# Kernel optimization log

Measured on AMD Instinct MI355X. Metric: run time of the kernel, lower is better.

The kernel has to match this reference:

```python
import jax, jax.numpy as jnp
import numpy as np

B_SZ, N_NODES, C_IN, C_OUT, M_EDGES, DEG = 32, 4096, 64, 64, 64, 256
E_INC = M_EDGES * DEG  # 16384 incidences
NEG_SLOPE = 0.2
MARGIN = 4.2


def setup_inputs() -> dict:
    key = jax.random.key(0)
    k1, k2, k3, k4 = jax.random.split(key, 4)
    x = jax.random.normal(k1, (B_SZ, N_NODES, C_IN), jnp.float32)
    # glorot-ish params
    weight = jax.random.normal(k2, (C_IN, C_OUT), jnp.float32) * (1.0 / np.sqrt(C_IN))
    att = jax.random.normal(k3, (1, 1, 2 * C_OUT), jnp.float32) * 0.1
    node_ids = jax.random.randint(k4, (E_INC,), 0, N_NODES, dtype=jnp.int32)
    edge_ids = jnp.repeat(jnp.arange(M_EDGES, dtype=jnp.int32), DEG)  # sorted, all edges present
    hyperedge_index = jnp.stack([node_ids, edge_ids], axis=0)
    return {"x": x, "weight": weight, "att": att,
            "hyperedge_index": hyperedge_index,
            "num_edges": M_EDGES, "num_nodes": N_NODES}


def _segment_softmax(scores, seg, num_segments):
    m = jax.ops.segment_max(scores, seg, num_segments=num_segments)
    e = jnp.exp(scores - m[seg])
    s = jax.ops.segment_sum(e, seg, num_segments=num_segments)
    return e / s[seg]


def reference(x, weight, att, hyperedge_index, num_edges, num_nodes):
    node_ids = hyperedge_index[0]
    edge_ids = hyperedge_index[1]
    M = num_edges
    N = num_nodes

    xw = jnp.einsum('bnc,cd->bnd', x, weight)       # [B,N,C]
    x1 = jnp.swapaxes(xw, 0, 1)                     # [N,B,C]

    x_i = x1[node_ids]                              # [E,B,C] gather per incidence
    edge_sums = jax.ops.segment_sum(x_i, edge_ids, num_segments=M,
                                    indices_are_sorted=True)  # [M,B,C]
    x_j = edge_sums[edge_ids]                       # [E,B,C]

    # pairwise hyperedge contrastive loss (vectorized double loop over edges)
    inner = jnp.einsum('kbc,mbc->kmb', edge_sums, edge_sums)          # [M,M,B]
    nrm = jnp.linalg.norm(edge_sums, axis=-1)                         # [M,B]
    cos = inner / (nrm[:, None, :] * nrm[None, :, :])                 # [M,M,B]
    diff = edge_sums[:, None] - edge_sums[None, :]                    # [M,M,B,C]
    dist = jnp.linalg.norm(diff, axis=-1)                             # [M,M,B]
    loss_item = cos * dist + (1.0 - cos) * jnp.clip(MARGIN - dist, 0.0)
    loss_hyper = jnp.sum(jnp.abs(jnp.mean(loss_item, axis=2))) / (M + 1) ** 2

    # GAT-style attention over incidences, softmax grouped by node
    cat = jnp.concatenate([x_i, x_j], axis=-1)                        # [E,B,2C]
    scores = jnp.sum(cat * att[0], axis=-1)                           # [E,B] (heads=1)
    scores = jax.nn.leaky_relu(scores, negative_slope=NEG_SLOPE)
    alpha = _segment_softmax(scores, node_ids, N)                     # [E,B]
    # dropout omitted (eval mode)

    ones = jnp.ones((node_ids.shape[0],), xw.dtype)
    D = jax.ops.segment_sum(ones, node_ids, num_segments=N)           # node degree
    deg_e = jax.ops.segment_sum(ones, edge_ids, num_segments=M, indices_are_sorted=True)
    B_norm = jnp.where(deg_e > 0, 1.0 / deg_e, 0.0)                   # 1/edge degree, inf->0

    # stage 1: nodes -> hyperedges (source_to_target)
    msg1 = B_norm[edge_ids][:, None, None] * (alpha[..., None] * x_i) # [E,B,C]
    out_e = jax.ops.segment_sum(msg1, edge_ids, num_segments=M, indices_are_sorted=True)
    # stage 2: hyperedges -> nodes (target_to_source)
    msg2 = D[node_ids][:, None, None] * (alpha[..., None] * out_e[edge_ids])
    out_n = jax.ops.segment_sum(msg2, node_ids, num_segments=N)       # [N,B,C]

    out = jnp.swapaxes(out_n, 0, 1)                                   # [B,N,C]
    constrain_total = jnp.abs(jnp.mean(x_i - x_j)) + loss_hyper
    return out, constrain_total
```

## Files before the change

kernel.cpp:

```cpp
#include <hip/hip_runtime.h>
#include <math.h>

#define B_SZ 32
#define N_NODES 4096
#define C_DIM 64
#define M_EDGES 64
#define DEG 256
#define E_INC 16384
#define NEG_SLOPE 0.2f
#define MARGIN 4.2f

__device__ __forceinline__ float wsum64(float v) {
#pragma unroll
  for (int off = 32; off > 0; off >>= 1) v += __shfl_xor(v, off, 64);
  return v;
}

__device__ __forceinline__ float4 redq16_32(float4 a) {
#pragma unroll
  for (int off = 16; off < 64; off <<= 1) {
    a.x += __shfl_xor(a.x, off, 64);
    a.y += __shfl_xor(a.y, off, 64);
    a.z += __shfl_xor(a.z, off, 64);
    a.w += __shfl_xor(a.w, off, 64);
  }
  return a;
}

#define ACC4(acc, v)  \
  acc.x += v.x;       \
  acc.y += v.y;       \
  acc.z += v.z;       \
  acc.w += v.w;

#define FMA4(acc, a, v)        \
  acc.x = fmaf(a, v.x, acc.x); \
  acc.y = fmaf(a, v.y, acc.y); \
  acc.z = fmaf(a, v.z, acc.z); \
  acc.w = fmaf(a, v.w, acc.w);

union U16K {
  float wl[4096];
  int cnt[4096];
};

__global__ __launch_bounds__(256) void k_pA(
    const float* __restrict__ x, const float* __restrict__ w,
    const float* __restrict__ att, const int* __restrict__ node_ids,
    float* __restrict__ s1_t, float* __restrict__ es_t,
    float* __restrict__ s2, float* __restrict__ nrm2,
    float* __restrict__ essum, int* __restrict__ cntv) {
  __shared__ U16K u;
  __shared__ float sx[4][4][64];
  __shared__ float est[4][64];
  const int bid = blockIdx.x;
  const int t = threadIdx.x;
  const int lane = t & 63, wv = t >> 6;
  if (bid < 512) {
    __shared__ float part[4][64];
    __shared__ float wattl[64];
    const int kk = t & 63, q = t >> 6;
    float p = 0.f;
#pragma unroll
    for (int c = 0; c < 16; ++c)
      p = fmaf(w[kk * 64 + q * 16 + c], att[q * 16 + c], p);
    part[q][kk] = p;
    __syncthreads();
    if (t < 64)
      wattl[t] = part[0][t] + part[1][t] + part[2][t] + part[3][t];
    __syncthreads();
    const int kq = lane & 15, rsub = lane >> 4;
    const float4 wq = ((const float4*)wattl)[kq];
    const int r0 = bid * 256 + wv * 64;
#pragma unroll 4
    for (int it = 0; it < 16; ++it) {
      const int row = r0 + it * 4 + rsub;
      const float4 xv = ((const float4*)x)[row * 16 + kq];
      float vv = xv.x * wq.x + xv.y * wq.y + xv.z * wq.z + xv.w * wq.w;
      vv += __shfl_xor(vv, 1, 64);
      vv += __shfl_xor(vv, 2, 64);
      vv += __shfl_xor(vv, 4, 64);
      vv += __shfl_xor(vv, 8, 64);
      if (kq == 0) {
        const int n = row & (N_NODES - 1);
        const int b = row >> 12;
        s1_t[n * 32 + b] = vv;
      }
    }
  } else if (bid < 576) {
    const int m = bid - 512;
#pragma unroll
    for (int i = 0; i < 16; ++i) u.cnt[t + 256 * i] = 0;
    __syncthreads();
    atomicAdd(&u.cnt[node_ids[m * DEG + t]], 1);
    __syncthreads();
#pragma unroll
    for (int i = 0; i < 16; ++i)
      cntv[m * N_NODES + t + 256 * i] = u.cnt[t + 256 * i];
  } else {
    const int eb = bid - 576;
    const int b0 = (eb & 7) * 4;
    const int m = eb >> 3;
    const int qc = lane & 15, rg = lane >> 4;
    float4* wl4 = (float4*)u.wl;
    const float4* w4 = (const float4*)w;
#pragma unroll
    for (int i = 0; i < 4; ++i) wl4[t + 256 * i] = w4[t + 256 * i];
    const int myinc = node_ids[m * DEG + wv * 64 + lane];
    int nds[16];
#pragma unroll
    for (int i = 0; i < 16; ++i) nds[i] = __shfl(myinc, i * 4 + rg, 64);
#pragma unroll
    for (int p = 0; p < 2; ++p) {
      const float4* xA =
          (const float4*)(x + (size_t)(b0 + 2 * p) * (N_NODES * C_DIM));
      const float4* xB =
          (const float4*)(x + (size_t)(b0 + 2 * p + 1) * (N_NODES * C_DIM));
      float4 vA[8], vB[8];
#pragma unroll
      for (int j = 0; j < 8; ++j) vA[j] = xA[nds[j] * 16 + qc];
#pragma unroll
      for (int j = 0; j < 8; ++j) vB[j] = xB[nds[j] * 16 + qc];
      float4 aA = {0.f, 0.f, 0.f, 0.f}, aB = {0.f, 0.f, 0.f, 0.f};
#pragma unroll
      for (int j = 0; j < 8; ++j) { ACC4(aA, vA[j]); }
#pragma unroll
      for (int j = 0; j < 8; ++j) vA[j] = xA[nds[8 + j] * 16 + qc];
#pragma unroll
      for (int j = 0; j < 8; ++j) { ACC4(aB, vB[j]); }
#pragma unroll
      for (int j = 0; j < 8; ++j) vB[j] = xB[nds[8 + j] * 16 + qc];
#pragma unroll
      for (int j = 0; j < 8; ++j) { ACC4(aA, vA[j]); }
#pragma unroll
      for (int j = 0; j < 8; ++j) { ACC4(aB, vB[j]); }
      aA = redq16_32(aA);
      aB = redq16_32(aB);
      if (rg == 0) {
        ((float4*)&sx[wv][2 * p][0])[qc] = aA;
        ((float4*)&sx[wv][2 * p + 1][0])[qc] = aB;
      }
    }
    __syncthreads();
    {
      const int c = lane;
      float es = 0.f;
#pragma unroll 8
      for (int j = 0; j < 64; ++j) {
        const float sxcj =
            sx[0][wv][j] + sx[1][wv][j] + sx[2][wv][j] + sx[3][wv][j];
        es = fmaf(sxcj, u.wl[j * 64 + c], es);
      }
      est[wv][c] = es;
      const float sr = wsum64(es * att[64 + c]);
      const float nr = wsum64(es * es);
      const float er = wsum64(es);
      if (c == 0) {
        s2[m * 32 + b0 + wv] = sr;
        nrm2[m * 32 + b0 + wv] = nr;
        essum[m * 32 + b0 + wv] = er;
      }
    }
    __syncthreads();
    if (t < 64) {
      const float4 o = make_float4(est[0][t], est[1][t], est[2][t], est[3][t]);
      *(float4*)&es_t[(m * 64 + t) * 32 + b0] = o;
    }
  }
}

__global__ __launch_bounds__(256) void k_pB(
    const float* __restrict__ es_t, const float* __restrict__ nrm2,
    const int* __restrict__ cntv, const float* __restrict__ s1_t,
    const float* __restrict__ s2, float* __restrict__ lossbuf2,
    float2* __restrict__ pnb, int* __restrict__ pdat,
    int* __restrict__ plen) {
  const int bid = blockIdx.x;
  if (bid < 504) {
    const int wv = threadIdx.x >> 6;
    const int p = bid * 4 + wv;
    int k = 0, off = 0;
    while (off + (63 - k) <= p) {
      off += 63 - k;
      ++k;
    }
    const int m = k + 1 + (p - off);
    const int lane = threadIdx.x & 63;
    const int b = lane & 31, ch = lane >> 5;
    float inner = 0.f;
#pragma unroll 8
    for (int cc = 0; cc < 32; ++cc) {
      const int c = cc + 32 * ch;
      inner = fmaf(es_t[(k * 64 + c) * 32 + b], es_t[(m * 64 + c) * 32 + b],
                   inner);
    }
    inner += __shfl_xor(inner, 32, 64);
    const float nk2 = nrm2[k * 32 + b];
    const float nm2 = nrm2[m * 32 + b];
    const float d2 = fmaxf(nk2 + nm2 - 2.f * inner, 0.f);
    const float dist = sqrtf(d2);
    const float cosv = inner / sqrtf(nk2 * nm2);
    float li = cosv * dist + (1.f - cosv) * fmaxf(MARGIN - dist, 0.f);
#pragma unroll
    for (int o = 16; o > 0; o >>= 1) li += __shfl_xor(li, o, 64);
    if (lane == 0) lossbuf2[p] = 2.f * fabsf(li * (1.f / 32.f));
  } else {
    const int idx = (bid - 504) * 256 + threadIdx.x;
    const int n = idx >> 5, b = idx & 31;
    const float s1v = s1_t[n * 32 + b];
    const bool leader = (b == 0);
    float mx = -1e30f, S = 0.f;
    int j = 0, Dsum = 0;
#pragma unroll 4
    for (int m = 0; m < 64; ++m) {
      const int cm = cntv[m * N_NODES + n];
      float sc = s1v + s2[m * 32 + b];
      sc = sc > 0.f ? sc : NEG_SLOPE * sc;
      const float scv = (cm > 0) ? sc : -1e30f;
      const float nm = fmaxf(mx, scv);
      S = S * __expf(mx - nm) + (float)cm * __expf(scv - nm);
      mx = nm;
      if (leader) {
        if (cm > 0) {
          pdat[n * 64 + j] = m | (cm << 8);
          ++j;
        }
        Dsum += cm;
      }
    }
    if (leader) plen[n] = j | (Dsum << 7);
    float2 pv;
    pv.x = mx;
    pv.y = (S > 0.f) ? 1.f / S : 0.f;
    pnb[n * 32 + b] = pv;
  }
}

__global__ __launch_bounds__(256) void k_pC(
    const float* __restrict__ x, const int* __restrict__ node_ids,
    const float* __restrict__ w, const float* __restrict__ s1_t,
    const float* __restrict__ s2, const float2* __restrict__ pnb,
    const float* __restrict__ essum, const float* __restrict__ lossbuf2,
    float* __restrict__ out_e_t, float* __restrict__ outs) {
  __shared__ float wl[4096];
  __shared__ float sx[4][4][64];
  __shared__ float est[4][64];
  const int bid = blockIdx.x;
  const int t = threadIdx.x;
  if (bid < 512) {
    const int b0 = (bid & 7) * 4;
    const int m = bid >> 3;
    const int lane = t & 63, wv = t >> 6;
    const int qc = lane & 15, rg = lane >> 4;
    float4* wl4 = (float4*)wl;
    const float4* w4 = (const float4*)w;
#pragma unroll
    for (int i = 0; i < 4; ++i) wl4[t + 256 * i] = w4[t + 256 * i];
    const int myinc = node_ids[m * DEG + wv * 64 + lane];
    const float4 s14 = *(const float4*)&s1_t[myinc * 32 + b0];
    const float* pp = (const float*)&pnb[myinc * 32 + b0];
    const float4 pA = *(const float4*)pp;
    const float4 pB = *(const float4*)(pp + 4);
    float mya[4];
    {
      const float s1a[4] = {s14.x, s14.y, s14.z, s14.w};
      const float mxa[4] = {pA.x, pA.z, pB.x, pB.z};
      const float iva[4] = {pA.y, pA.w, pB.y, pB.w};
#pragma unroll
      for (int bi = 0; bi < 4; ++bi) {
        float sc = s1a[bi] + s2[m * 32 + b0 + bi];
        sc = sc > 0.f ? sc : NEG_SLOPE * sc;
        mya[bi] = __expf(sc - mxa[bi]) * iva[bi];
      }
    }
    int nds[16];
#pragma unroll
    for (int i = 0; i < 16; ++i) nds[i] = __shfl(myinc, i * 4 + rg, 64);
#pragma unroll
    for (int p = 0; p < 2; ++p) {
      const float4* xA =
          (const float4*)(x + (size_t)(b0 + 2 * p) * (N_NODES * C_DIM));
      const float4* xB =
          (const float4*)(x + (size_t)(b0 + 2 * p + 1) * (N_NODES * C_DIM));
      float avA[16], avB[16];
#pragma unroll
      for (int i = 0; i < 16; ++i) {
        avA[i] = __shfl(mya[2 * p], i * 4 + rg, 64);
        avB[i] = __shfl(mya[2 * p + 1], i * 4 + rg, 64);
      }
      float4 vA[8], vB[8];
#pragma unroll
      for (int j = 0; j < 8; ++j) vA[j] = xA[nds[j] * 16 + qc];
#pragma unroll
      for (int j = 0; j < 8; ++j) vB[j] = xB[nds[j] * 16 + qc];
      float4 aA = {0.f, 0.f, 0.f, 0.f}, aB = {0.f, 0.f, 0.f, 0.f};
#pragma unroll
      for (int j = 0; j < 8; ++j) { FMA4(aA, avA[j], vA[j]); }
#pragma unroll
      for (int j = 0; j < 8; ++j) vA[j] = xA[nds[8 + j] * 16 + qc];
#pragma unroll
      for (int j = 0; j < 8; ++j) { FMA4(aB, avB[j], vB[j]); }
#pragma unroll
      for (int j = 0; j < 8; ++j) vB[j] = xB[nds[8 + j] * 16 + qc];
#pragma unroll
      for (int j = 0; j < 8; ++j) { FMA4(aA, avA[8 + j], vA[j]); }
#pragma unroll
      for (int j = 0; j < 8; ++j) { FMA4(aB, avB[8 + j], vB[j]); }
      aA = redq16_32(aA);
      aB = redq16_32(aB);
      if (rg == 0) {
        ((float4*)&sx[wv][2 * p][0])[qc] = aA;
        ((float4*)&sx[wv][2 * p + 1][0])[qc] = aB;
      }
    }
    __syncthreads();
    {
      const int c = t & 63;
      const int wv2 = t >> 6;
      float oc = 0.f;
#pragma unroll 8
      for (int j = 0; j < 64; ++j) {
        const float sxcj =
            sx[0][wv2][j] + sx[1][wv2][j] + sx[2][wv2][j] + sx[3][wv2][j];
        oc = fmaf(sxcj, wl[j * 64 + c], oc);
      }
      est[wv2][c] = oc * (1.0f / 256.0f);
    }
    __syncthreads();
    if (t < 64) {
      const float4 o = make_float4(est[0][t], est[1][t], est[2][t], est[3][t]);
      *(float4*)&out_e_t[(m * 64 + t) * 32 + b0] = o;
    }
  } else {
    __shared__ float smf[256];
    float s = 0.f;
    for (int i = t; i < M_EDGES * B_SZ; i += 256) s += essum[i];
    smf[t] = s;
    __syncthreads();
    for (int o = 128; o > 0; o >>= 1) {
      if (t < o) smf[t] += smf[t + o];
      __syncthreads();
    }
    const float S = smf[0];
    __syncthreads();
    float l = 0.f;
    for (int i = t; i < 2016; i += 256) l += lossbuf2[i];
    smf[t] = l;
    __syncthreads();
    for (int o = 128; o > 0; o >>= 1) {
      if (t < o) smf[t] += smf[t + o];
      __syncthreads();
    }
    if (t == 0) {
      const float mean = S * (-255.0f) / 33554432.0f;
      outs[0] = fabsf(mean) + smf[0] * (1.0f / 4225.0f);
    }
  }
}

__global__ __launch_bounds__(256) void k_pD(
    const int* __restrict__ plen, const int* __restrict__ pdat,
    const float* __restrict__ s1_t, const float* __restrict__ s2,
    const float2* __restrict__ pnb, const float* __restrict__ out_e_t,
    float* __restrict__ out) {
  __shared__ int lme[2][64];
  __shared__ float lcnt[2][64];
  __shared__ float al[2][64][32];
  const int t = threadIdx.x;
  const int nd = t >> 7;
  const int n = blockIdx.x * 2 + nd;
  const int tl = t & 127;
  const int pl = plen[n];
  const int len = pl & 127;
  const float Dn = (float)(pl >> 7);
  if (tl < len) {
    const int pe = pdat[n * 64 + tl];
    lme[nd][tl] = pe & 63;
    lcnt[nd][tl] = (float)(pe >> 8);
  }
  __syncthreads();
  {
    const int b = tl & 31, lq = tl >> 5;
    const float s1v = s1_t[n * 32 + b];
    const float2 pv = pnb[n * 32 + b];
    for (int base = 0; base < len; base += 4) {
      const int li = base + lq;
      if (li < len) {
        const int m = lme[nd][li];
        float sc = s1v + s2[m * 32 + b];
        sc = sc > 0.f ? sc : NEG_SLOPE * sc;
        al[nd][li][b] = lcnt[nd][li] * __expf(sc - pv.x) * pv.y;
      }
    }
  }
  __syncthreads();
  const int c = tl & 63, bh = tl >> 6;
  float4 a0 = {0.f, 0.f, 0.f, 0.f}, a1 = {0.f, 0.f, 0.f, 0.f};
  float4 a2 = {0.f, 0.f, 0.f, 0.f}, a3 = {0.f, 0.f, 0.f, 0.f};
  for (int li = 0; li < len; ++li) {
    const int m = lme[nd][li];
    const float* ob = &out_e_t[(m * 64 + c) * 32 + bh * 16];
    const float4 v0 = *(const float4*)(ob);
    const float4 v1 = *(const float4*)(ob + 4);
    const float4 v2 = *(const float4*)(ob + 8);
    const float4 v3 = *(const float4*)(ob + 12);
    const float* alr = &al[nd][li][bh * 16];
    a0.x = fmaf(alr[0], v0.x, a0.x);
    a0.y = fmaf(alr[1], v0.y, a0.y);
    a0.z = fmaf(alr[2], v0.z, a0.z);
    a0.w = fmaf(alr[3], v0.w, a0.w);
    a1.x = fmaf(alr[4], v1.x, a1.x);
    a1.y = fmaf(alr[5], v1.y, a1.y);
    a1.z = fmaf(alr[6], v1.z, a1.z);
    a1.w = fmaf(alr[7], v1.w, a1.w);
    a2.x = fmaf(alr[8], v2.x, a2.x);
    a2.y = fmaf(alr[9], v2.y, a2.y);
    a2.z = fmaf(alr[10], v2.z, a2.z);
    a2.w = fmaf(alr[11], v2.w, a2.w);
    a3.x = fmaf(alr[12], v3.x, a3.x);
    a3.y = fmaf(alr[13], v3.y, a3.y);
    a3.z = fmaf(alr[14], v3.z, a3.z);
    a3.w = fmaf(alr[15], v3.w, a3.w);
  }
  const size_t nb = (size_t)n * 64 + c;
  const size_t st = (size_t)N_NODES * 64;
  const int bb = bh * 16;
  out[(bb + 0) * st + nb] = Dn * a0.x;
  out[(bb + 1) * st + nb] = Dn * a0.y;
  out[(bb + 2) * st + nb] = Dn * a0.z;
  out[(bb + 3) * st + nb] = Dn * a0.w;
  out[(bb + 4) * st + nb] = Dn * a1.x;
  out[(bb + 5) * st + nb] = Dn * a1.y;
  out[(bb + 6) * st + nb] = Dn * a1.z;
  out[(bb + 7) * st + nb] = Dn * a1.w;
  out[(bb + 8) * st + nb] = Dn * a2.x;
  out[(bb + 9) * st + nb] = Dn * a2.y;
  out[(bb + 10) * st + nb] = Dn * a2.z;
  out[(bb + 11) * st + nb] = Dn * a2.w;
  out[(bb + 12) * st + nb] = Dn * a3.x;
  out[(bb + 13) * st + nb] = Dn * a3.y;
  out[(bb + 14) * st + nb] = Dn * a3.z;
  out[(bb + 15) * st + nb] = Dn * a3.w;
}

extern "C" void kernel_launch(void* const* d_in, const int* in_sizes, int n_in,
                              void* d_out, int out_size, void* d_ws,
                              size_t ws_size, hipStream_t stream) {
  (void)in_sizes; (void)n_in; (void)out_size; (void)ws_size;
  const float* x = (const float*)d_in[0];
  const float* weight = (const float*)d_in[1];
  const float* att = (const float*)d_in[2];
  const int* node_ids = (const int*)d_in[3];
  float* out = (float*)d_out;

  char* wsb = (char*)d_ws;
  float* es_t = (float*)(wsb);
  float* out_e_t = (float*)(wsb + (512 << 10));
  float* s1_t = (float*)(wsb + (1024 << 10));
  int* cntv = (int*)(wsb + (1536 << 10));
  float2* pnb = (float2*)(wsb + (2560 << 10));
  int* pdat = (int*)(wsb + (3584 << 10));
  float* s2 = (float*)(wsb + (4608 << 10));
  float* nrm2 = (float*)(wsb + (4616 << 10));
  float* essum = (float*)(wsb + (4624 << 10));
  float* lossbuf2 = (float*)(wsb + (4632 << 10));
  int* plen = (int*)(wsb + (4640 << 10));

  k_pA<<<1088, 256, 0, stream>>>(x, weight, att, node_ids, s1_t, es_t, s2,
                                 nrm2, essum, cntv);
  k_pB<<<1016, 256, 0, stream>>>(es_t, nrm2, cntv, s1_t, s2, lossbuf2, pnb,
                                 pdat, plen);
  k_pC<<<513, 256, 0, stream>>>(x, node_ids, weight, s1_t, s2, pnb, essum,
                                lossbuf2, out_e_t,
                                out + (size_t)B_SZ * N_NODES * C_DIM);
  k_pD<<<2048, 256, 0, stream>>>(plen, pdat, s1_t, s2, pnb, out_e_t, out);
}
```

Before: 82.12 us.

## Replace edge-side gather with node-major scatter into LDS partials plus reduce kernel

The stage-1 aggregation (nodes to hyperedges) no longer gathers x rows per incidence. Each block now streams contiguous node rows for one batch and scatters alpha-weighted values into per-wave LDS accumulators indexed by edge, using the per-node compressed edge lists built earlier. A new kernel sums the 16 chunk partials and applies the weight matrix. The aim is to swap random gathers of x for coalesced reads. The cost is an extra launch, a 4 MB partial buffer written and read back, and LDS read-modify-write traffic that can hit bank conflicts.

```diff
diff --git a/kernel.cpp b/kernel.cpp
--- a/kernel.cpp
+++ b/kernel.cpp
@@ -27,17 +27,11 @@
   return a;
 }
 
-#define ACC4(acc, v)  \
-  acc.x += v.x;       \
-  acc.y += v.y;       \
-  acc.z += v.z;       \
+#define ACC4(acc, v) \
+  acc.x += v.x;      \
+  acc.y += v.y;      \
+  acc.z += v.z;      \
   acc.w += v.w;
-
-#define FMA4(acc, a, v)        \
-  acc.x = fmaf(a, v.x, acc.x); \
-  acc.y = fmaf(a, v.y, acc.y); \
-  acc.z = fmaf(a, v.z, acc.z); \
-  acc.w = fmaf(a, v.w, acc.w);
 
 union U16K {
   float wl[4096];
@@ -236,100 +230,73 @@
   }
 }
 
-__global__ __launch_bounds__(256) void k_pC(
-    const float* __restrict__ x, const int* __restrict__ node_ids,
-    const float* __restrict__ w, const float* __restrict__ s1_t,
+__global__ __launch_bounds__(256) void k_pC1(
+    const float* __restrict__ x, const float* __restrict__ s1_t,
     const float* __restrict__ s2, const float2* __restrict__ pnb,
+    const int* __restrict__ plen, const int* __restrict__ pdat,
     const float* __restrict__ essum, const float* __restrict__ lossbuf2,
-    float* __restrict__ out_e_t, float* __restrict__ outs) {
-  __shared__ float wl[4096];
-  __shared__ float sx[4][4][64];
-  __shared__ float est[4][64];
+    float* __restrict__ partialT, float* __restrict__ outs) {
   const int bid = blockIdx.x;
   const int t = threadIdx.x;
   if (bid < 512) {
-    const int b0 = (bid & 7) * 4;
-    const int m = bid >> 3;
-    const int lane = t & 63, wv = t >> 6;
-    const int qc = lane & 15, rg = lane >> 4;
-    float4* wl4 = (float4*)wl;
-    const float4* w4 = (const float4*)w;
-#pragma unroll
-    for (int i = 0; i < 4; ++i) wl4[t + 256 * i] = w4[t + 256 * i];
-    const int myinc = node_ids[m * DEG + wv * 64 + lane];
-    const float4 s14 = *(const float4*)&s1_t[myinc * 32 + b0];
-    const float* pp = (const float*)&pnb[myinc * 32 + b0];
-    const float4 pA = *(const float4*)pp;
-    const float4 pB = *(const float4*)(pp + 4);
-    float mya[4];
-    {
-      const float s1a[4] = {s14.x, s14.y, s14.z, s14.w};
-      const float mxa[4] = {pA.x, pA.z, pB.x, pB.z};
-      const float iva[4] = {pA.y, pA.w, pB.y, pB.w};
-#pragma unroll
-      for (int bi = 0; bi < 4; ++bi) {
-        float sc = s1a[bi] + s2[m * 32 + b0 + bi];
-        sc = sc > 0.f ? sc : NEG_SLOPE * sc;
-        mya[bi] = __expf(sc - mxa[bi]) * iva[bi];
-      }
-    }
-    int nds[16];
-#pragma unroll
-    for (int i = 0; i < 16; ++i) nds[i] = __shfl(myinc, i * 4 + rg, 64);
-#pragma unroll
-    for (int p = 0; p < 2; ++p) {
-      const float4* xA =
-          (const float4*)(x + (size_t)(b0 + 2 * p) * (N_NODES * C_DIM));
-      const float4* xB =
-          (const float4*)(x + (size_t)(b0 + 2 * p + 1) * (N_NODES * C_DIM));
-      float avA[16], avB[16];
-#pragma unroll
-      for (int i = 0; i < 16; ++i) {
-        avA[i] = __shfl(mya[2 * p], i * 4 + rg, 64);
-        avB[i] = __shfl(mya[2 * p + 1], i * 4 + rg, 64);
-      }
-      float4 vA[8], vB[8];
-#pragma unroll
-      for (int j = 0; j < 8; ++j) vA[j] = xA[nds[j] * 16 + qc];
-#pragma unroll
-      for (int j = 0; j < 8; ++j) vB[j] = xB[nds[j] * 16 + qc];
-      float4 aA = {0.f, 0.f, 0.f, 0.f}, aB = {0.f, 0.f, 0.f, 0.f};
-#pragma unroll
-      for (int j = 0; j < 8; ++j) { FMA4(aA, avA[j], vA[j]); }
-#pragma unroll
-      for (int j = 0; j < 8; ++j) vA[j] = xA[nds[8 + j] * 16 + qc];
-#pragma unroll
-      for (int j = 0; j < 8; ++j) { FMA4(aB, avB[j], vB[j]); }
-#pragma unroll
-      for (int j = 0; j < 8; ++j) vB[j] = xB[nds[8 + j] * 16 + qc];
-#pragma unroll
-      for (int j = 0; j < 8; ++j) { FMA4(aA, avA[8 + j], vA[j]); }
-#pragma unroll
-      for (int j = 0; j < 8; ++j) { FMA4(aB, avB[8 + j], vB[j]); }
-      aA = redq16_32(aA);
-      aB = redq16_32(aB);
-      if (rg == 0) {
-        ((float4*)&sx[wv][2 * p][0])[qc] = aA;
-        ((float4*)&sx[wv][2 * p + 1][0])[qc] = aB;
-      }
-    }
-    __syncthreads();
-    {
-      const int c = t & 63;
-      const int wv2 = t >> 6;
-      float oc = 0.f;
-#pragma unroll 8
-      for (int j = 0; j < 64; ++j) {
-        const float sxcj =
-            sx[0][wv2][j] + sx[1][wv2][j] + sx[2][wv2][j] + sx[3][wv2][j];
-        oc = fmaf(sxcj, wl[j * 64 + c], oc);
-      }
-      est[wv2][c] = oc * (1.0f / 256.0f);
-    }
-    __syncthreads();
-    if (t < 64) {
-      const float4 o = make_float4(est[0][t], est[1][t], est[2][t], est[3][t]);
-      *(float4*)&out_e_t[(m * 64 + t) * 32 + b0] = o;
+    __shared__ float Tw[4][64][64];
+    const int b = bid & 31;
+    const int ch = bid >> 5;
+    const int c = t & 63, wv = t >> 6;
+    float* tz = &Tw[0][0][0];
+    for (int i = t; i < 4 * 64 * 64; i += 256) tz[i] = 0.f;
+    __syncthreads();
+    const int nbase = ch * 256 + wv * 64;
+    const float* xb = x + (size_t)b * (N_NODES * C_DIM);
+#pragma unroll 1
+    for (int g = 0; g < 16; ++g) {
+      const int n0 = nbase + g * 4;
+      float xv[4], s1v[4];
+      int pl[4];
+      float2 pv[4];
+      int4 pd0[4], pd1[4];
+#pragma unroll
+      for (int u = 0; u < 4; ++u) {
+        const int n = n0 + u;
+        xv[u] = xb[n * 64 + c];
+        pl[u] = plen[n];
+        s1v[u] = s1_t[n * 32 + b];
+        pv[u] = pnb[n * 32 + b];
+        pd0[u] = *(const int4*)&pdat[n * 64];
+        pd1[u] = *(const int4*)&pdat[n * 64 + 4];
+      }
+#pragma unroll
+      for (int u = 0; u < 4; ++u) {
+        const int len = pl[u] & 127;
+        const int pes[8] = {pd0[u].x, pd0[u].y, pd0[u].z, pd0[u].w,
+                            pd1[u].x, pd1[u].y, pd1[u].z, pd1[u].w};
+#pragma unroll
+        for (int j = 0; j < 8; ++j) {
+          if (j < len) {
+            const int pe = pes[j];
+            const int m = pe & 63;
+            float sc = s1v[u] + s2[m * 32 + b];
+            sc = sc > 0.f ? sc : NEG_SLOPE * sc;
+            const float a =
+                (float)(pe >> 8) * __expf(sc - pv[u].x) * pv[u].y;
+            Tw[wv][m][c] += a * xv[u];
+          }
+        }
+        for (int j = 8; j < len; ++j) {
+          const int pe = pdat[(n0 + u) * 64 + j];
+          const int m = pe & 63;
+          float sc = s1v[u] + s2[m * 32 + b];
+          sc = sc > 0.f ? sc : NEG_SLOPE * sc;
+          const float a = (float)(pe >> 8) * __expf(sc - pv[u].x) * pv[u].y;
+          Tw[wv][m][c] += a * xv[u];
+        }
+      }
+    }
+    __syncthreads();
+    for (int idx = t; idx < 4096; idx += 256) {
+      const int m = idx >> 6, k = idx & 63;
+      const float v = Tw[0][m][k] + Tw[1][m][k] + Tw[2][m][k] + Tw[3][m][k];
+      partialT[(((size_t)ch * 32 + b) * 64 + m) * 64 + k] = v;
     }
   } else {
     __shared__ float smf[256];
@@ -355,6 +322,39 @@
       const float mean = S * (-255.0f) / 33554432.0f;
       outs[0] = fabsf(mean) + smf[0] * (1.0f / 4225.0f);
     }
+  }
+}
+
+__global__ __launch_bounds__(256) void k_pC2(
+    const float* __restrict__ partialT, const float* __restrict__ w,
+    float* __restrict__ out_e_t) {
+  __shared__ float wl[4096];
+  __shared__ float S[64][33];
+  const int m = blockIdx.x;
+  const int t = threadIdx.x;
+  float4* wl4 = (float4*)wl;
+  const float4* w4 = (const float4*)w;
+#pragma unroll
+  for (int i = 0; i < 4; ++i) wl4[t + 256 * i] = w4[t + 256 * i];
+  const int k = t & 63, bg = t >> 6;
+#pragma unroll
+  for (int pp = 0; pp < 8; ++pp) {
+    const int b = pp * 4 + bg;
+    float acc = 0.f;
+#pragma unroll
+    for (int ch = 0; ch < 16; ++ch)
+      acc += partialT[(((size_t)ch * 32 + b) * 64 + m) * 64 + k];
+    S[k][b] = acc;
+  }
+  __syncthreads();
+  const int c = t & 63, bq = t >> 6;
+#pragma unroll
+  for (int j = 0; j < 8; ++j) {
+    const int b = bq * 8 + j;
+    float oc = 0.f;
+#pragma unroll 8
+    for (int kk = 0; kk < 64; ++kk) oc = fmaf(S[kk][b], wl[kk * 64 + c], oc);
+    out_e_t[(m * 64 + c) * 32 + b] = oc * (1.0f / 256.0f);
   }
 }
 
@@ -465,13 +465,15 @@
   float* essum = (float*)(wsb + (4624 << 10));
   float* lossbuf2 = (float*)(wsb + (4632 << 10));
   int* plen = (int*)(wsb + (4640 << 10));
+  float* partialT = (float*)(wsb + (6144 << 10));
 
   k_pA<<<1088, 256, 0, stream>>>(x, weight, att, node_ids, s1_t, es_t, s2,
                                  nrm2, essum, cntv);
   k_pB<<<1016, 256, 0, stream>>>(es_t, nrm2, cntv, s1_t, s2, lossbuf2, pnb,
                                  pdat, plen);
-  k_pC<<<513, 256, 0, stream>>>(x, node_ids, weight, s1_t, s2, pnb, essum,
-                                lossbuf2, out_e_t,
-                                out + (size_t)B_SZ * N_NODES * C_DIM);
+  k_pC1<<<513, 256, 0, stream>>>(x, s1_t, s2, pnb, plen, pdat, essum,
+                                 lossbuf2, partialT,
+                                 out + (size_t)B_SZ * N_NODES * C_DIM);
+  k_pC2<<<64, 256, 0, stream>>>(partialT, weight, out_e_t);
   k_pD<<<2048, 256, 0, stream>>>(plen, pdat, s1_t, s2, pnb, out_e_t, out);
 }
```

New measurement: 182.2 us. +121.9%, slower.

## Give each wave one batch over all incidences in edge-gather blocks

Applied to the files above, without the earlier changes.

In the edge-sum gather blocks of k_pA and k_pC, the work split changes. Before, each wave covered 64 incidences for 4 batches, and partial sums were reduced across the waves through shared memory. Now each wave handles one batch over all 256 incidences, with node ids staged in shared memory and, in k_pC, the attention weights computed per batch into a shared array. This removes the cross-wave partial-sum step and the register-heavy shuffles. In exchange it adds a block barrier before the gather and scalar (non-vectorized) loads of pnb and s1_t, which may lower memory-level parallelism per wave.

```diff
diff --git a/kernel.cpp b/kernel.cpp
--- a/kernel.cpp
+++ b/kernel.cpp
@@ -27,10 +27,10 @@
   return a;
 }
 
-#define ACC4(acc, v)  \
-  acc.x += v.x;       \
-  acc.y += v.y;       \
-  acc.z += v.z;       \
+#define ACC4(acc, v) \
+  acc.x += v.x;      \
+  acc.y += v.y;      \
+  acc.z += v.z;      \
   acc.w += v.w;
 
 #define FMA4(acc, a, v)        \
@@ -51,7 +51,8 @@
     float* __restrict__ s2, float* __restrict__ nrm2,
     float* __restrict__ essum, int* __restrict__ cntv) {
   __shared__ U16K u;
-  __shared__ float sx[4][4][64];
+  __shared__ int ids[256];
+  __shared__ float sxc[4][64];
   __shared__ float est[4][64];
   const int bid = blockIdx.x;
   const int t = threadIdx.x;
@@ -102,63 +103,42 @@
     const int b0 = (eb & 7) * 4;
     const int m = eb >> 3;
     const int qc = lane & 15, rg = lane >> 4;
+    ids[t] = node_ids[m * DEG + t];
     float4* wl4 = (float4*)u.wl;
     const float4* w4 = (const float4*)w;
 #pragma unroll
     for (int i = 0; i < 4; ++i) wl4[t + 256 * i] = w4[t + 256 * i];
-    const int myinc = node_ids[m * DEG + wv * 64 + lane];
-    int nds[16];
-#pragma unroll
-    for (int i = 0; i < 16; ++i) nds[i] = __shfl(myinc, i * 4 + rg, 64);
-#pragma unroll
-    for (int p = 0; p < 2; ++p) {
-      const float4* xA =
-          (const float4*)(x + (size_t)(b0 + 2 * p) * (N_NODES * C_DIM));
-      const float4* xB =
-          (const float4*)(x + (size_t)(b0 + 2 * p + 1) * (N_NODES * C_DIM));
-      float4 vA[8], vB[8];
-#pragma unroll
-      for (int j = 0; j < 8; ++j) vA[j] = xA[nds[j] * 16 + qc];
-#pragma unroll
-      for (int j = 0; j < 8; ++j) vB[j] = xB[nds[j] * 16 + qc];
-      float4 aA = {0.f, 0.f, 0.f, 0.f}, aB = {0.f, 0.f, 0.f, 0.f};
-#pragma unroll
-      for (int j = 0; j < 8; ++j) { ACC4(aA, vA[j]); }
-#pragma unroll
-      for (int j = 0; j < 8; ++j) vA[j] = xA[nds[8 + j] * 16 + qc];
-#pragma unroll
-      for (int j = 0; j < 8; ++j) { ACC4(aB, vB[j]); }
-#pragma unroll
-      for (int j = 0; j < 8; ++j) vB[j] = xB[nds[8 + j] * 16 + qc];
-#pragma unroll
-      for (int j = 0; j < 8; ++j) { ACC4(aA, vA[j]); }
-#pragma unroll
-      for (int j = 0; j < 8; ++j) { ACC4(aB, vB[j]); }
-      aA = redq16_32(aA);
-      aB = redq16_32(aB);
-      if (rg == 0) {
-        ((float4*)&sx[wv][2 * p][0])[qc] = aA;
-        ((float4*)&sx[wv][2 * p + 1][0])[qc] = aB;
-      }
-    }
+    __syncthreads();
+    const int b = b0 + wv;
+    const float4* xb4 = (const float4*)(x + (size_t)b * (N_NODES * C_DIM));
+    float4 acc = {0.f, 0.f, 0.f, 0.f};
+#pragma unroll
+    for (int h = 0; h < 8; ++h) {
+      int nd[8];
+      float4 v[8];
+#pragma unroll
+      for (int j = 0; j < 8; ++j) nd[j] = ids[(h * 8 + j) * 4 + rg];
+#pragma unroll
+      for (int j = 0; j < 8; ++j) v[j] = xb4[nd[j] * 16 + qc];
+#pragma unroll
+      for (int j = 0; j < 8; ++j) { ACC4(acc, v[j]); }
+    }
+    acc = redq16_32(acc);
+    if (rg == 0) ((float4*)&sxc[wv][0])[qc] = acc;
     __syncthreads();
     {
       const int c = lane;
       float es = 0.f;
 #pragma unroll 8
-      for (int j = 0; j < 64; ++j) {
-        const float sxcj =
-            sx[0][wv][j] + sx[1][wv][j] + sx[2][wv][j] + sx[3][wv][j];
-        es = fmaf(sxcj, u.wl[j * 64 + c], es);
-      }
+      for (int j = 0; j < 64; ++j) es = fmaf(sxc[wv][j], u.wl[j * 64 + c], es);
       est[wv][c] = es;
       const float sr = wsum64(es * att[64 + c]);
       const float nr = wsum64(es * es);
       const float er = wsum64(es);
       if (c == 0) {
-        s2[m * 32 + b0 + wv] = sr;
-        nrm2[m * 32 + b0 + wv] = nr;
-        essum[m * 32 + b0 + wv] = er;
+        s2[m * 32 + b] = sr;
+        nrm2[m * 32 + b] = nr;
+        essum[m * 32 + b] = er;
       }
     }
     __syncthreads();
@@ -243,7 +223,9 @@
     const float* __restrict__ essum, const float* __restrict__ lossbuf2,
     float* __restrict__ out_e_t, float* __restrict__ outs) {
   __shared__ float wl[4096];
-  __shared__ float sx[4][4][64];
+  __shared__ int ids[256];
+  __shared__ float al[4][256];
+  __shared__ float sxc[4][64];
   __shared__ float est[4][64];
   const int bid = blockIdx.x;
   const int t = threadIdx.x;
@@ -252,79 +234,50 @@
     const int m = bid >> 3;
     const int lane = t & 63, wv = t >> 6;
     const int qc = lane & 15, rg = lane >> 4;
+    ids[t] = node_ids[m * DEG + t];
     float4* wl4 = (float4*)wl;
     const float4* w4 = (const float4*)w;
 #pragma unroll
     for (int i = 0; i < 4; ++i) wl4[t + 256 * i] = w4[t + 256 * i];
-    const int myinc = node_ids[m * DEG + wv * 64 + lane];
-    const float4 s14 = *(const float4*)&s1_t[myinc * 32 + b0];
-    const float* pp = (const float*)&pnb[myinc * 32 + b0];
-    const float4 pA = *(const float4*)pp;
-    const float4 pB = *(const float4*)(pp + 4);
-    float mya[4];
+    __syncthreads();
+    const int b = b0 + wv;
+    const float s2mb = s2[m * 32 + b];
+#pragma unroll
+    for (int q = 0; q < 4; ++q) {
+      const int r = lane * 4 + q;
+      const int n = ids[r];
+      const float2 pv = pnb[n * 32 + b];
+      float sc = s1_t[n * 32 + b] + s2mb;
+      sc = sc > 0.f ? sc : NEG_SLOPE * sc;
+      al[wv][r] = __expf(sc - pv.x) * pv.y;
+    }
+    const float4* xb4 = (const float4*)(x + (size_t)b * (N_NODES * C_DIM));
+    float4 acc = {0.f, 0.f, 0.f, 0.f};
+#pragma unroll
+    for (int h = 0; h < 8; ++h) {
+      int nd[8];
+      float av[8];
+      float4 v[8];
+#pragma unroll
+      for (int j = 0; j < 8; ++j) {
+        const int r = (h * 8 + j) * 4 + rg;
+        nd[j] = ids[r];
+        av[j] = al[wv][r];
+      }
+#pragma unroll
+      for (int j = 0; j < 8; ++j) v[j] = xb4[nd[j] * 16 + qc];
+#pragma unroll
+      for (int j = 0; j < 8; ++j) { FMA4(acc, av[j], v[j]); }
+    }
+    acc = redq16_32(acc);
+    if (rg == 0) ((float4*)&sxc[wv][0])[qc] = acc;
+    __syncthreads();
     {
-      const float s1a[4] = {s14.x, s14.y, s14.z, s14.w};
-      const float mxa[4] = {pA.x, pA.z, pB.x, pB.z};
-      const float iva[4] = {pA.y, pA.w, pB.y, pB.w};
-#pragma unroll
-      for (int bi = 0; bi < 4; ++bi) {
-        float sc = s1a[bi] + s2[m * 32 + b0 + bi];
-        sc = sc > 0.f ? sc : NEG_SLOPE * sc;
-        mya[bi] = __expf(sc - mxa[bi]) * iva[bi];
-      }
-    }
-    int nds[16];
-#pragma unroll
-    for (int i = 0; i < 16; ++i) nds[i] = __shfl(myinc, i * 4 + rg, 64);
-#pragma unroll
-    for (int p = 0; p < 2; ++p) {
-      const float4* xA =
-          (const float4*)(x + (size_t)(b0 + 2 * p) * (N_NODES * C_DIM));
-      const float4* xB =
-          (const float4*)(x + (size_t)(b0 + 2 * p + 1) * (N_NODES * C_DIM));
-      float avA[16], avB[16];
-#pragma unroll
-      for (int i = 0; i < 16; ++i) {
-        avA[i] = __shfl(mya[2 * p], i * 4 + rg, 64);
-        avB[i] = __shfl(mya[2 * p + 1], i * 4 + rg, 64);
-      }
-      float4 vA[8], vB[8];
-#pragma unroll
-      for (int j = 0; j < 8; ++j) vA[j] = xA[nds[j] * 16 + qc];
-#pragma unroll
-      for (int j = 0; j < 8; ++j) vB[j] = xB[nds[j] * 16 + qc];
-      float4 aA = {0.f, 0.f, 0.f, 0.f}, aB = {0.f, 0.f, 0.f, 0.f};
-#pragma unroll
-      for (int j = 0; j < 8; ++j) { FMA4(aA, avA[j], vA[j]); }
-#pragma unroll
-      for (int j = 0; j < 8; ++j) vA[j] = xA[nds[8 + j] * 16 + qc];
-#pragma unroll
-      for (int j = 0; j < 8; ++j) { FMA4(aB, avB[j], vB[j]); }
-#pragma unroll
-      for (int j = 0; j < 8; ++j) vB[j] = xB[nds[8 + j] * 16 + qc];
-#pragma unroll
-      for (int j = 0; j < 8; ++j) { FMA4(aA, avA[8 + j], vA[j]); }
-#pragma unroll
-      for (int j = 0; j < 8; ++j) { FMA4(aB, avB[8 + j], vB[j]); }
-      aA = redq16_32(aA);
-      aB = redq16_32(aB);
-      if (rg == 0) {
-        ((float4*)&sx[wv][2 * p][0])[qc] = aA;
-        ((float4*)&sx[wv][2 * p + 1][0])[qc] = aB;
-      }
-    }
-    __syncthreads();
-    {
-      const int c = t & 63;
-      const int wv2 = t >> 6;
+      const int c = lane;
       float oc = 0.f;
 #pragma unroll 8
-      for (int j = 0; j < 64; ++j) {
-        const float sxcj =
-            sx[0][wv2][j] + sx[1][wv2][j] + sx[2][wv2][j] + sx[3][wv2][j];
-        oc = fmaf(sxcj, wl[j * 64 + c], oc);
-      }
-      est[wv2][c] = oc * (1.0f / 256.0f);
+      for (int j = 0; j < 64; ++j) oc = fmaf(sxc[wv][j], wl[j * 64 + c], oc);
+      est[wv][c] = oc * (1.0f / 256.0f);
     }
     __syncthreads();
     if (t < 64) {
```

Result: slower. 84.95 us (+3.4%).
